# Optimization experiments

Hardware: AMD Instinct MI355X
Metric: run time of the kernel (lower is better)

The kernel has to match this reference:

```python
import jax, jax.numpy as jnp
import numpy as np
from jax import lax

B, T, X_DIM, HID, VOCAB = 64, 32, 512, 512, 10000


def setup_inputs() -> dict:
    key = jax.random.key(0)
    ks = jax.random.split(key, 20)
    s = 0.1
    inp = {
        "x": jax.random.normal(ks[0], (B, T, X_DIM), dtype=jnp.float32),
        "h": jax.random.normal(ks[1], (B, HID), dtype=jnp.float32),
        "c": jax.random.normal(ks[2], (B, HID), dtype=jnp.float32),
        "W_hi": jax.random.normal(ks[3], (HID, HID), dtype=jnp.float32) * s,
        "W_xi": jax.random.normal(ks[4], (X_DIM, HID), dtype=jnp.float32) * s,
        "b_i": jnp.zeros((HID,), dtype=jnp.float32),
        "W_hf": jax.random.normal(ks[5], (HID, HID), dtype=jnp.float32) * s,
        "W_xf": jax.random.normal(ks[6], (X_DIM, HID), dtype=jnp.float32) * s,
        "b_f": jnp.zeros((HID,), dtype=jnp.float32),
        "W_ho": jax.random.normal(ks[7], (HID, HID), dtype=jnp.float32) * s,
        "W_xo": jax.random.normal(ks[8], (X_DIM, HID), dtype=jnp.float32) * s,
        "b_o": jnp.zeros((HID,), dtype=jnp.float32),
        "W_hz": jax.random.normal(ks[9], (HID, HID), dtype=jnp.float32) * s,
        "W_xz": jax.random.normal(ks[10], (X_DIM, HID), dtype=jnp.float32) * s,
        "b_z": jnp.zeros((HID,), dtype=jnp.float32),
        # per-timestep Linear(hidden, vocab) bank: [T, HID, VOCAB] (y = h @ W + b)
        "W_lin": jax.random.normal(ks[11], (T, HID, VOCAB), dtype=jnp.float32) * 0.02,
        "b_lin": jnp.zeros((T, VOCAB), dtype=jnp.float32),
        # global embedding_layer: vocab -> x_dim
        "emb": jax.random.normal(ks[12], (VOCAB, X_DIM), dtype=jnp.float32) * 0.02,
    }
    return inp


def reference(x, h, c, W_hi, W_xi, b_i, W_hf, W_xf, b_f,
              W_ho, W_xo, b_o, W_hz, W_xz, b_z, W_lin, b_lin, emb):
    T_ = x.shape[1]
    # Faithful to the source: step 0 uses linear_list[0], then the loop over
    # t in range(T-1) uses linear_list[t] -> indices [0, 0, 1, ..., T-2].
    lin_idx = jnp.concatenate([jnp.zeros((1,), jnp.int32), jnp.arange(T_ - 1, dtype=jnp.int32)])
    Wl = W_lin[lin_idx]  # [T, HID, VOCAB]
    bl = b_lin[lin_idx]  # [T, VOCAB]

    def cell(x_in, h, c):
        i = jax.nn.sigmoid(h @ W_hi + x_in @ W_xi + b_i)
        f = jax.nn.sigmoid(h @ W_hf + x_in @ W_xf + b_f)
        o = jax.nn.sigmoid(h @ W_ho + x_in @ W_xo + b_o)
        z = jnp.tanh(h @ W_hz + x_in @ W_xz + b_z)
        c = i * z + f * c
        h = o * jnp.tanh(c)
        return h, c

    def step(carry, wb):
        h, c, x_in = carry
        Wt, bt = wb
        h, c = cell(x_in, h, c)
        y = jax.nn.softmax(h @ Wt + bt, axis=-1)  # [B, VOCAB]
        tok = jnp.argmax(y, axis=-1)              # [B]
        x_next = emb[tok]                         # [B, X_DIM]
        return (h, c, x_next), (y, c)

    # Only x[:, 0] is consumed (decoder feeds back argmax embeddings).
    (_, _, _), (ys, cs) = lax.scan(step, (h, c, x[:, 0]), (Wl, bl))
    outputs = jnp.transpose(ys, (1, 0, 2))      # [B, T, VOCAB]
    cell_states = jnp.transpose(cs, (1, 0, 2))  # [B, T, HID]
    return outputs, cell_states
```

## Files before the change

kernel.cpp:

```cpp
#include <hip/hip_runtime.h>
#include <hip/hip_bf16.h>
#include <stdint.h>

#define BB 64
#define TT 32
#define HID 512
#define XD  512
#define NV  10000

#define GRID   512
#define NCELL  128
#define VB     32
#define NLOG   313
#define LOGB   128
#define NORMB  441

typedef __bf16 bf16x8 __attribute__((ext_vector_type(8)));
typedef float  f32x4  __attribute__((ext_vector_type(4)));
typedef unsigned u32x4 __attribute__((ext_vector_type(4)));

__device__ inline void split2(float w, __bf16& hi, __bf16& lo) {
  hi = (__bf16)w;
  lo = (__bf16)(w - (float)hi);
}

__device__ inline unsigned long long shflxor64(unsigned long long v, int m) {
  unsigned lo = (unsigned)(v & 0xFFFFFFFFull);
  unsigned hi = (unsigned)(v >> 32);
  lo = __shfl_xor(lo, m);
  hi = __shfl_xor(hi, m);
  return ((unsigned long long)hi << 32) | lo;
}

__device__ inline unsigned long long packkey(float f, int v) {
  unsigned ub = __float_as_uint(f);
  unsigned key = (ub & 0x80000000u) ? ~ub : (ub | 0x80000000u);
  return ((unsigned long long)key << 32) | (unsigned)(0xFFFFFFFFu - (unsigned)v);
}

__device__ inline void st_wt16(void* addr, u32x4 d) {
  asm volatile("global_store_dwordx4 %0, %1, off sc0 sc1"
               :: "v"(addr), "v"(d) : "memory");
}

__device__ inline void spinP(int* base, int target) {
  if (threadIdx.x < 64) {
    int lane = threadIdx.x;
    int s;
    do {
      int v = 0;
      if (lane < 16)
        v = __hip_atomic_load(base + lane * 16, __ATOMIC_RELAXED,
                              __HIP_MEMORY_SCOPE_AGENT);
      #pragma unroll
      for (int m = 1; m < 16; m <<= 1) v += __shfl_xor(v, m);
      s = __shfl(v, 0);
      if (s < target) __builtin_amdgcn_s_sleep(1);
    } while (s < target);
  }
  __syncthreads();
}
__device__ inline void publish(int* base) {
  asm volatile("s_waitcnt vmcnt(0)" ::: "memory");
  __syncthreads();
  if (threadIdx.x == 0)
    __hip_atomic_fetch_add(base + (blockIdx.x & 15) * 16, 1,
                           __ATOMIC_RELAXED, __HIP_MEMORY_SCOPE_AGENT);
}

struct Params {
  const float *x, *emb;
  const float *Whi, *Whf, *Who, *Whz;
  const float *Wxi, *Wxf, *Wxo, *Wxz;
  const float *bi, *bfg, *bo, *bz;
  const float *W_lin, *b_lin;
  float* out;
  char* hb;
  char* xb;
  float* c_ws;
  float* psum;
  unsigned long long* pmax;
  float* inv;
  int* ctr;
};

__device__ inline void loadH(const char* hb, int tt, int row, int kk,
                             bf16x8& ah, bf16x8& al) {
  size_t off = (((size_t)tt * 128 + (kk >> 2)) * 64 + row) * 16;
  uint4 v0 = *(const uint4*)(hb + off);
  uint4 v1 = *(const uint4*)(hb + off + 1024);
  union { unsigned u[4]; bf16x8 v; } A, B;
  A.u[0] = v0.x; A.u[1] = v0.y; A.u[2] = v1.x; A.u[3] = v1.y;
  B.u[0] = v0.z; B.u[1] = v0.w; B.u[2] = v1.z; B.u[3] = v1.w;
  ah = A.v; al = B.v;
}

struct SMCell { __bf16 Ch[16][1042]; __bf16 Cl[16][1042]; float pre[64][17]; };
struct SMLog  { __bf16 Bh[32][522];  __bf16 Bl[32][522]; };
union SMU { SMCell c; SMLog l; };

__global__ __launch_bounds__(256) void k_init(
    const float* __restrict__ h0, const float* __restrict__ c0,
    char* __restrict__ hb, float* __restrict__ c_ws, int* __restrict__ ctrs) {
  int i = blockIdx.x * 256 + threadIdx.x;
  int row = i >> 9, k = i & 511, g = k >> 2, q = k & 3;
  float h = h0[i];
  __bf16 hi, lo; split2(h, hi, lo);
  char* base = hb + (((size_t)g) * 64 + row) * 16;
  ((unsigned short*)base)[q]       = __builtin_bit_cast(unsigned short, hi);
  ((unsigned short*)(base + 8))[q] = __builtin_bit_cast(unsigned short, lo);
  c_ws[i] = c0[i];
  if (i < 3 * TT * 256) ctrs[i] = 0;
}

__global__ __launch_bounds__(256, 2) void k_main(Params p) {
  __shared__ SMU sm;
  __shared__ float red_s[4];
  __shared__ unsigned long long red_m[4];
  __shared__ unsigned sh_tok;
  const int bid = blockIdx.x, tid = threadIdx.x;
  const int lane = tid & 63, wid = tid >> 6;

  int* cd0 = p.ctr;
  int* ld0 = p.ctr + TT * 256;
  int* rn0 = p.ctr + 2 * TT * 256;

  if (bid < NCELL) {
    const int n0 = bid * 4;
    const float* WH[4] = {p.Whi, p.Whf, p.Who, p.Whz};
    const float* WX[4] = {p.Wxi, p.Wxf, p.Wxo, p.Wxz};

    #pragma unroll
    for (int i2 = 0; i2 < 16; i2++) {
      int e = tid + i2 * 256;
      int k = e >> 2, g = e & 3;
      const float* src = (k < HID) ? (WH[g] + (size_t)k * HID + n0)
                                   : (WX[g] + (size_t)(k - HID) * HID + n0);
      float4 w = *(const float4*)src;
      #pragma unroll
      for (int j = 0; j < 4; j++) {
        __bf16 hi, lo; split2(((const float*)&w)[j], hi, lo);
        sm.c.Ch[g * 4 + j][k] = hi;
        sm.c.Cl[g * 4 + j][k] = lo;
      }
    }
    __syncthreads();

    const int row  = wid * 16 + (lane & 15);
    const int brow = lane & 15;

    for (int t = 0; t < TT; t++) {
      if (t > 0) spinP(cd0 + (t - 1) * 256, NCELL);

      f32x4 accA = {0.f, 0.f, 0.f, 0.f};
      f32x4 accB = {0.f, 0.f, 0.f, 0.f};

      #pragma unroll
      for (int ks = 0; ks < 16; ks++) {
        int kk = ks * 32 + (lane >> 4) * 8;
        bf16x8 ah, al;
        loadH(p.hb, t, row, kk, ah, al);
        bf16x8 bh = *(const bf16x8*)&sm.c.Ch[brow][kk];
        bf16x8 bl = *(const bf16x8*)&sm.c.Cl[brow][kk];
        accA = __builtin_amdgcn_mfma_f32_16x16x32_bf16(ah, bh, accA, 0, 0, 0);
        accB = __builtin_amdgcn_mfma_f32_16x16x32_bf16(ah, bl, accB, 0, 0, 0);
        accB = __builtin_amdgcn_mfma_f32_16x16x32_bf16(al, bh, accB, 0, 0, 0);
        accA = __builtin_amdgcn_mfma_f32_16x16x32_bf16(al, bl, accA, 0, 0, 0);
      }

      if (t == 0) {
        const float* xrow = p.x + (size_t)row * TT * XD;
        #pragma unroll
        for (int ks = 16; ks < 32; ks++) {
          int kk = ks * 32 + (lane >> 4) * 8;
          const float* xp = xrow + (kk - HID);
          float4 w0 = *(const float4*)(xp);
          float4 w1 = *(const float4*)(xp + 4);
          bf16x8 ah, al;
          #pragma unroll
          for (int j = 0; j < 4; j++) {
            __bf16 hi, lo;
            split2(((const float*)&w0)[j], hi, lo); ah[j] = hi; al[j] = lo;
            split2(((const float*)&w1)[j], hi, lo); ah[4 + j] = hi; al[4 + j] = lo;
          }
          bf16x8 bh = *(const bf16x8*)&sm.c.Ch[brow][kk];
          bf16x8 bl = *(const bf16x8*)&sm.c.Cl[brow][kk];
          accA = __builtin_amdgcn_mfma_f32_16x16x32_bf16(ah, bh, accA, 0, 0, 0);
          accB = __builtin_amdgcn_mfma_f32_16x16x32_bf16(ah, bl, accB, 0, 0, 0);
          accB = __builtin_amdgcn_mfma_f32_16x16x32_bf16(al, bh, accB, 0, 0, 0);
          accA = __builtin_amdgcn_mfma_f32_16x16x32_bf16(al, bl, accA, 0, 0, 0);
        }
      } else {
        spinP(rn0 + (t - 1) * 256, BB);
        #pragma unroll
        for (int ks = 16; ks < 32; ks++) {
          int kk = ks * 32 + (lane >> 4) * 8;
          bf16x8 ah, al;
          loadH(p.xb, t - 1, row, kk - 512, ah, al);
          bf16x8 bh = *(const bf16x8*)&sm.c.Ch[brow][kk];
          bf16x8 bl = *(const bf16x8*)&sm.c.Cl[brow][kk];
          accA = __builtin_amdgcn_mfma_f32_16x16x32_bf16(ah, bh, accA, 0, 0, 0);
          accB = __builtin_amdgcn_mfma_f32_16x16x32_bf16(ah, bl, accB, 0, 0, 0);
          accB = __builtin_amdgcn_mfma_f32_16x16x32_bf16(al, bh, accB, 0, 0, 0);
          accA = __builtin_amdgcn_mfma_f32_16x16x32_bf16(al, bl, accA, 0, 0, 0);
        }
      }

      #pragma unroll
      for (int j = 0; j < 4; j++)
        sm.c.pre[wid * 16 + (lane >> 4) * 4 + j][lane & 15] = accA[j] + accB[j];
      __syncthreads();

      float cnv; int rl, nn;
      {
        int rloc = tid >> 2, q = tid & 3;
        int n = n0 + q;
        float pi = sm.c.pre[rloc][q]      + p.bi[n];
        float pf = sm.c.pre[rloc][4 + q]  + p.bfg[n];
        float pq = sm.c.pre[rloc][8 + q]  + p.bo[n];
        float pz = sm.c.pre[rloc][12 + q] + p.bz[n];
        float ig = 1.f / (1.f + expf(-pi));
        float fg = 1.f / (1.f + expf(-pf));
        float og = 1.f / (1.f + expf(-pq));
        float zg = tanhf(pz);
        float cp = p.c_ws[rloc * HID + n];
        float cn = ig * zg + fg * cp;
        float hn = og * tanhf(cn);
        __bf16 hh, hl; split2(hn, hh, hl);
        unsigned hhu = (unsigned)__builtin_bit_cast(unsigned short, hh);
        unsigned hlu = (unsigned)__builtin_bit_cast(unsigned short, hl);
        unsigned hi1 = __shfl_down(hhu, 1), hi2 = __shfl_down(hhu, 2),
                 hi3 = __shfl_down(hhu, 3);
        unsigned lo1 = __shfl_down(hlu, 1), lo2 = __shfl_down(hlu, 2),
                 lo3 = __shfl_down(hlu, 3);
        if (q == 0) {
          u32x4 d = { hhu | (hi1 << 16), hi2 | (hi3 << 16),
                      hlu | (lo1 << 16), lo2 | (lo3 << 16) };
          st_wt16(p.hb + (((size_t)(t + 1) * 128 + bid) * 64 + rloc) * 16, d);
        }
        cnv = cn; rl = rloc; nn = n;
      }
      publish(cd0 + t * 256);
      p.c_ws[rl * HID + nn] = cnv;
      p.out[(size_t)BB * TT * NV + (size_t)rl * TT * HID + (size_t)t * HID + nn] = cnv;
    }
    return;
  }

  if (bid < NORMB) {
    const int lb = bid - LOGB;
    const int v0 = lb * VB;
    const int row = wid * 16 + (lane & 15);

    float bcar[2];
    float evp[2][4];

    auto stageW = [&](int widx) {
      const float* W = p.W_lin + (size_t)widx * HID * NV;
      float4 v[16];
      #pragma unroll
      for (int i2 = 0; i2 < 16; i2++) {
        int e = tid + i2 * 256;
        int k = e >> 3, pp = e & 7;
        v[i2] = *(const float4*)(W + (size_t)k * NV + v0 + pp * 4);
      }
      const float* bn = p.b_lin + (size_t)widx * NV;
      bcar[0] = bn[v0 + (lane & 15)];
      bcar[1] = bn[v0 + 16 + (lane & 15)];
      #pragma unroll
      for (int i2 = 0; i2 < 16; i2++) {
        int e = tid + i2 * 256;
        int k = e >> 3, pp = e & 7;
        #pragma unroll
        for (int j = 0; j < 4; j++) {
          __bf16 hi, lo; split2(((const float*)&v[i2])[j], hi, lo);
          sm.l.Bh[pp * 4 + j][k] = hi;
          sm.l.Bl[pp * 4 + j][k] = lo;
        }
      }
    };

    stageW(0);

    for (int t = 0; t < TT; t++) {
      spinP(cd0 + t * 256, NCELL);

      f32x4 acc[2][2] = {};
      #pragma unroll
      for (int ks = 0; ks < 16; ks++) {
        int kk = ks * 32 + (lane >> 4) * 8;
        bf16x8 ah, al;
        loadH(p.hb, t + 1, row, kk, ah, al);
        #pragma unroll
        for (int vt = 0; vt < 2; vt++) {
          int rrow = vt * 16 + (lane & 15);
          bf16x8 bh = *(const bf16x8*)&sm.l.Bh[rrow][kk];
          bf16x8 bl = *(const bf16x8*)&sm.l.Bl[rrow][kk];
          acc[vt][0] = __builtin_amdgcn_mfma_f32_16x16x32_bf16(ah, bh, acc[vt][0], 0, 0, 0);
          acc[vt][1] = __builtin_amdgcn_mfma_f32_16x16x32_bf16(ah, bl, acc[vt][1], 0, 0, 0);
          acc[vt][1] = __builtin_amdgcn_mfma_f32_16x16x32_bf16(al, bh, acc[vt][1], 0, 0, 0);
          acc[vt][0] = __builtin_amdgcn_mfma_f32_16x16x32_bf16(al, bl, acc[vt][0], 0, 0, 0);
        }
      }

      float ev[2][4];
      float rsum[4] = {0.f, 0.f, 0.f, 0.f};
      unsigned long long rmax[4] = {0ULL, 0ULL, 0ULL, 0ULL};
      #pragma unroll
      for (int vt = 0; vt < 2; vt++) {
        int v = v0 + vt * 16 + (lane & 15);
        bool ok = (v < NV);
        float bb = ok ? bcar[vt] : 0.f;
        #pragma unroll
        for (int j = 0; j < 4; j++) {
          float logit = acc[vt][0][j] + acc[vt][1][j] + bb;
          float e = ok ? expf(logit) : 0.f;
          ev[vt][j] = e;
          rsum[j] += e;
          if (ok) {
            unsigned long long pk = packkey(logit, v);
            if (pk > rmax[j]) rmax[j] = pk;
          }
        }
      }

      #pragma unroll
      for (int off = 1; off < 16; off <<= 1) {
        #pragma unroll
        for (int j = 0; j < 4; j++) {
          rsum[j] += __shfl_xor(rsum[j], off);
          unsigned long long o = shflxor64(rmax[j], off);
          if (o > rmax[j]) rmax[j] = o;
        }
      }
      if ((lane & 15) == 0) {
        int rbase = wid * 16 + (lane >> 4) * 4;
        union { float f[4]; u32x4 u; } S;
        S.f[0] = rsum[0]; S.f[1] = rsum[1]; S.f[2] = rsum[2]; S.f[3] = rsum[3];
        st_wt16(&p.psum[((size_t)t * NLOG + lb) * 64 + rbase], S.u);
        u32x4 M0 = { (unsigned)rmax[0], (unsigned)(rmax[0] >> 32),
                     (unsigned)rmax[1], (unsigned)(rmax[1] >> 32) };
        u32x4 M1 = { (unsigned)rmax[2], (unsigned)(rmax[2] >> 32),
                     (unsigned)rmax[3], (unsigned)(rmax[3] >> 32) };
        st_wt16(&p.pmax[((size_t)t * NLOG + lb) * 64 + rbase], M0);
        st_wt16(&p.pmax[((size_t)t * NLOG + lb) * 64 + rbase + 2], M1);
      }
      publish(ld0 + t * 256);

      if (t < TT - 1) stageW(t);

      if (t > 0) {
        float invr[4];
        #pragma unroll
        for (int j = 0; j < 4; j++)
          invr[j] = p.inv[(size_t)(t - 1) * BB + wid * 16 + (lane >> 4) * 4 + j];
        #pragma unroll
        for (int vt = 0; vt < 2; vt++) {
          int v = v0 + vt * 16 + (lane & 15);
          if (v < NV) {
            #pragma unroll
            for (int j = 0; j < 4; j++) {
              int r = wid * 16 + (lane >> 4) * 4 + j;
              p.out[(size_t)r * TT * NV + (size_t)(t - 1) * NV + v] = evp[vt][j] * invr[j];
            }
          }
        }
      }
      #pragma unroll
      for (int vt = 0; vt < 2; vt++)
        #pragma unroll
        for (int j = 0; j < 4; j++) evp[vt][j] = ev[vt][j];
    }

    spinP(rn0 + (TT - 1) * 256, BB);
    float invr[4];
    #pragma unroll
    for (int j = 0; j < 4; j++)
      invr[j] = p.inv[(size_t)(TT - 1) * BB + wid * 16 + (lane >> 4) * 4 + j];
    #pragma unroll
    for (int vt = 0; vt < 2; vt++) {
      int v = v0 + vt * 16 + (lane & 15);
      if (v < NV) {
        #pragma unroll
        for (int j = 0; j < 4; j++) {
          int r = wid * 16 + (lane >> 4) * 4 + j;
          p.out[(size_t)r * TT * NV + (size_t)(TT - 1) * NV + v] = evp[vt][j] * invr[j];
        }
      }
    }
    return;
  }

  if (bid < NORMB + BB) {
    const int r = bid - NORMB;
    for (int t = 0; t < TT; t++) {
      spinP(ld0 + t * 256, NLOG);

      float s = 0.f; unsigned long long m = 0ULL;
      for (int i = tid; i < NLOG; i += 256) {
        s += p.psum[((size_t)t * NLOG + i) * 64 + r];
        unsigned long long v = p.pmax[((size_t)t * NLOG + i) * 64 + r];
        if (v > m) m = v;
      }
      #pragma unroll
      for (int off = 1; off < 64; off <<= 1) {
        s += __shfl_xor(s, off);
        unsigned long long o = shflxor64(m, off);
        if (o > m) m = o;
      }
      if (lane == 0) { red_s[wid] = s; red_m[wid] = m; }
      __syncthreads();
      if (tid == 0) {
        s = red_s[0] + red_s[1] + red_s[2] + red_s[3];
        m = red_m[0];
        if (red_m[1] > m) m = red_m[1];
        if (red_m[2] > m) m = red_m[2];
        if (red_m[3] > m) m = red_m[3];
        sh_tok = 0xFFFFFFFFu - (unsigned)(m & 0xFFFFFFFFull);
        __hip_atomic_store(&p.inv[(size_t)t * BB + r], 1.0f / s,
                           __ATOMIC_RELAXED, __HIP_MEMORY_SCOPE_AGENT);
      }
      __syncthreads();

      unsigned tokv = sh_tok;
      if (tid < 128) {
        float4 w = *(const float4*)(p.emb + (size_t)tokv * XD + tid * 4);
        unsigned h[4], l[4];
        #pragma unroll
        for (int j = 0; j < 4; j++) {
          __bf16 hi, lo; split2(((const float*)&w)[j], hi, lo);
          h[j] = (unsigned)__builtin_bit_cast(unsigned short, hi);
          l[j] = (unsigned)__builtin_bit_cast(unsigned short, lo);
        }
        u32x4 d = { h[0] | (h[1] << 16), h[2] | (h[3] << 16),
                    l[0] | (l[1] << 16), l[2] | (l[3] << 16) };
        st_wt16(p.xb + (((size_t)t * 128 + tid) * 64 + r) * 16, d);
      }
      publish(rn0 + t * 256);
      __syncthreads();
    }
    return;
  }
}

extern "C" void kernel_launch(void* const* d_in, const int* in_sizes, int n_in,
                              void* d_out, int out_size, void* d_ws, size_t ws_size,
                              hipStream_t stream) {
  const float* x     = (const float*)d_in[0];
  const float* h0    = (const float*)d_in[1];
  const float* c0    = (const float*)d_in[2];
  const float* W_hi  = (const float*)d_in[3];
  const float* W_xi  = (const float*)d_in[4];
  const float* b_i   = (const float*)d_in[5];
  const float* W_hf  = (const float*)d_in[6];
  const float* W_xf  = (const float*)d_in[7];
  const float* b_f   = (const float*)d_in[8];
  const float* W_ho  = (const float*)d_in[9];
  const float* W_xo  = (const float*)d_in[10];
  const float* b_o   = (const float*)d_in[11];
  const float* W_hz  = (const float*)d_in[12];
  const float* W_xz  = (const float*)d_in[13];
  const float* b_z   = (const float*)d_in[14];
  const float* W_lin = (const float*)d_in[15];
  const float* b_lin = (const float*)d_in[16];
  const float* emb   = (const float*)d_in[17];

  float* out = (float*)d_out;
  char* ws = (char*)d_ws;
  char*   hb   = ws;
  char*   xb   = ws + 4325376;
  float*  c_ws = (float*)(ws + 8519680);
  float*  psum = (float*)(ws + 8650752);
  unsigned long long* pmax = (unsigned long long*)(ws + 11214848);
  float*  inv  = (float*)(ws + 16343040);
  int*    ctrs = (int*)(ws + 16351232);

  k_init<<<128, 256, 0, stream>>>(h0, c0, hb, c_ws, ctrs);

  Params P;
  P.x = x; P.emb = emb;
  P.Whi = W_hi; P.Whf = W_hf; P.Who = W_ho; P.Whz = W_hz;
  P.Wxi = W_xi; P.Wxf = W_xf; P.Wxo = W_xo; P.Wxz = W_xz;
  P.bi = b_i; P.bfg = b_f; P.bo = b_o; P.bz = b_z;
  P.W_lin = W_lin; P.b_lin = b_lin;
  P.out = out;
  P.hb = hb; P.xb = xb; P.c_ws = c_ws;
  P.psum = psum; P.pmax = pmax; P.inv = inv;
  P.ctr = ctrs;

  k_main<<<GRID, 256, 0, stream>>>(P);
}
```

Baseline: 818.3 us.

## Publish argmax tokens and gather embeddings in cell blocks; prefetch W_lin before publish

```diff
diff --git a/kernel.cpp b/kernel.cpp
--- a/kernel.cpp
+++ b/kernel.cpp
@@ -76,10 +76,10 @@
   const float *W_lin, *b_lin;
   float* out;
   char* hb;
-  char* xb;
   float* c_ws;
   float* psum;
   unsigned long long* pmax;
+  unsigned* tok;
   float* inv;
   int* ctr;
 };
@@ -117,7 +117,6 @@
   __shared__ SMU sm;
   __shared__ float red_s[4];
   __shared__ unsigned long long red_m[4];
-  __shared__ unsigned sh_tok;
   const int bid = blockIdx.x, tid = threadIdx.x;
   const int lane = tid & 63, wid = tid >> 6;
 
@@ -168,42 +167,34 @@
         accA = __builtin_amdgcn_mfma_f32_16x16x32_bf16(al, bl, accA, 0, 0, 0);
       }
 
+      const float* xrow;
       if (t == 0) {
-        const float* xrow = p.x + (size_t)row * TT * XD;
-        #pragma unroll
-        for (int ks = 16; ks < 32; ks++) {
-          int kk = ks * 32 + (lane >> 4) * 8;
-          const float* xp = xrow + (kk - HID);
-          float4 w0 = *(const float4*)(xp);
-          float4 w1 = *(const float4*)(xp + 4);
-          bf16x8 ah, al;
-          #pragma unroll
-          for (int j = 0; j < 4; j++) {
-            __bf16 hi, lo;
-            split2(((const float*)&w0)[j], hi, lo); ah[j] = hi; al[j] = lo;
-            split2(((const float*)&w1)[j], hi, lo); ah[4 + j] = hi; al[4 + j] = lo;
-          }
-          bf16x8 bh = *(const bf16x8*)&sm.c.Ch[brow][kk];
-          bf16x8 bl = *(const bf16x8*)&sm.c.Cl[brow][kk];
-          accA = __builtin_amdgcn_mfma_f32_16x16x32_bf16(ah, bh, accA, 0, 0, 0);
-          accB = __builtin_amdgcn_mfma_f32_16x16x32_bf16(ah, bl, accB, 0, 0, 0);
-          accB = __builtin_amdgcn_mfma_f32_16x16x32_bf16(al, bh, accB, 0, 0, 0);
-          accA = __builtin_amdgcn_mfma_f32_16x16x32_bf16(al, bl, accA, 0, 0, 0);
-        }
+        xrow = p.x + (size_t)row * TT * XD;
       } else {
         spinP(rn0 + (t - 1) * 256, BB);
-        #pragma unroll
-        for (int ks = 16; ks < 32; ks++) {
-          int kk = ks * 32 + (lane >> 4) * 8;
-          bf16x8 ah, al;
-          loadH(p.xb, t - 1, row, kk - 512, ah, al);
-          bf16x8 bh = *(const bf16x8*)&sm.c.Ch[brow][kk];
-          bf16x8 bl = *(const bf16x8*)&sm.c.Cl[brow][kk];
-          accA = __builtin_amdgcn_mfma_f32_16x16x32_bf16(ah, bh, accA, 0, 0, 0);
-          accB = __builtin_amdgcn_mfma_f32_16x16x32_bf16(ah, bl, accB, 0, 0, 0);
-          accB = __builtin_amdgcn_mfma_f32_16x16x32_bf16(al, bh, accB, 0, 0, 0);
-          accA = __builtin_amdgcn_mfma_f32_16x16x32_bf16(al, bl, accA, 0, 0, 0);
-        }
+        unsigned tokv = p.tok[(size_t)(t - 1) * BB + row];
+        xrow = p.emb + (size_t)tokv * XD;
+      }
+
+      #pragma unroll
+      for (int ks = 16; ks < 32; ks++) {
+        int kk = ks * 32 + (lane >> 4) * 8;
+        const float* xp = xrow + (kk - HID);
+        float4 w0 = *(const float4*)(xp);
+        float4 w1 = *(const float4*)(xp + 4);
+        bf16x8 ah, al;
+        #pragma unroll
+        for (int j = 0; j < 4; j++) {
+          __bf16 hi, lo;
+          split2(((const float*)&w0)[j], hi, lo); ah[j] = hi; al[j] = lo;
+          split2(((const float*)&w1)[j], hi, lo); ah[4 + j] = hi; al[4 + j] = lo;
+        }
+        bf16x8 bh = *(const bf16x8*)&sm.c.Ch[brow][kk];
+        bf16x8 bl = *(const bf16x8*)&sm.c.Cl[brow][kk];
+        accA = __builtin_amdgcn_mfma_f32_16x16x32_bf16(ah, bh, accA, 0, 0, 0);
+        accB = __builtin_amdgcn_mfma_f32_16x16x32_bf16(ah, bl, accB, 0, 0, 0);
+        accB = __builtin_amdgcn_mfma_f32_16x16x32_bf16(al, bh, accB, 0, 0, 0);
+        accA = __builtin_amdgcn_mfma_f32_16x16x32_bf16(al, bl, accA, 0, 0, 0);
       }
 
       #pragma unroll
@@ -255,15 +246,16 @@
     float bcar[2];
     float evp[2][4];
 
-    auto stageW = [&](int widx) {
+    auto issueW = [&](int widx, float4* v) {
       const float* W = p.W_lin + (size_t)widx * HID * NV;
-      float4 v[16];
       #pragma unroll
       for (int i2 = 0; i2 < 16; i2++) {
         int e = tid + i2 * 256;
         int k = e >> 3, pp = e & 7;
         v[i2] = *(const float4*)(W + (size_t)k * NV + v0 + pp * 4);
       }
+    };
+    auto convertW = [&](int widx, float4* v) {
       const float* bn = p.b_lin + (size_t)widx * NV;
       bcar[0] = bn[v0 + (lane & 15)];
       bcar[1] = bn[v0 + 16 + (lane & 15)];
@@ -280,10 +272,15 @@
       }
     };
 
-    stageW(0);
+    {
+      float4 v[16];
+      issueW(0, v);
+      convertW(0, v);
+    }
 
     for (int t = 0; t < TT; t++) {
       spinP(cd0 + t * 256, NCELL);
+      asm volatile("s_waitcnt vmcnt(0)" ::: "memory");
 
       f32x4 acc[2][2] = {};
       #pragma unroll
@@ -345,9 +342,19 @@
         st_wt16(&p.pmax[((size_t)t * NLOG + lb) * 64 + rbase], M0);
         st_wt16(&p.pmax[((size_t)t * NLOG + lb) * 64 + rbase + 2], M1);
       }
-      publish(ld0 + t * 256);
-
-      if (t < TT - 1) stageW(t);
+      float4 v[16];
+      if (t < TT - 1) {
+        issueW(t, v);
+        asm volatile("s_waitcnt vmcnt(16)" ::: "memory");
+      } else {
+        asm volatile("s_waitcnt vmcnt(0)" ::: "memory");
+      }
+      __syncthreads();
+      if (tid == 0)
+        __hip_atomic_fetch_add(ld0 + t * 256 + (bid & 15) * 16, 1,
+                               __ATOMIC_RELAXED, __HIP_MEMORY_SCOPE_AGENT);
+
+      if (t < TT - 1) convertW(t, v);
 
       if (t > 0) {
         float invr[4];
@@ -416,25 +423,11 @@
         if (red_m[1] > m) m = red_m[1];
         if (red_m[2] > m) m = red_m[2];
         if (red_m[3] > m) m = red_m[3];
-        sh_tok = 0xFFFFFFFFu - (unsigned)(m & 0xFFFFFFFFull);
+        __hip_atomic_store(&p.tok[(size_t)t * BB + r],
+                           0xFFFFFFFFu - (unsigned)(m & 0xFFFFFFFFull),
+                           __ATOMIC_RELAXED, __HIP_MEMORY_SCOPE_AGENT);
         __hip_atomic_store(&p.inv[(size_t)t * BB + r], 1.0f / s,
                            __ATOMIC_RELAXED, __HIP_MEMORY_SCOPE_AGENT);
-      }
-      __syncthreads();
-
-      unsigned tokv = sh_tok;
-      if (tid < 128) {
-        float4 w = *(const float4*)(p.emb + (size_t)tokv * XD + tid * 4);
-        unsigned h[4], l[4];
-        #pragma unroll
-        for (int j = 0; j < 4; j++) {
-          __bf16 hi, lo; split2(((const float*)&w)[j], hi, lo);
-          h[j] = (unsigned)__builtin_bit_cast(unsigned short, hi);
-          l[j] = (unsigned)__builtin_bit_cast(unsigned short, lo);
-        }
-        u32x4 d = { h[0] | (h[1] << 16), h[2] | (h[3] << 16),
-                    l[0] | (l[1] << 16), l[2] | (l[3] << 16) };
-        st_wt16(p.xb + (((size_t)t * 128 + tid) * 64 + r) * 16, d);
       }
       publish(rn0 + t * 256);
       __syncthreads();
@@ -468,12 +461,12 @@
   float* out = (float*)d_out;
   char* ws = (char*)d_ws;
   char*   hb   = ws;
-  char*   xb   = ws + 4325376;
-  float*  c_ws = (float*)(ws + 8519680);
-  float*  psum = (float*)(ws + 8650752);
-  unsigned long long* pmax = (unsigned long long*)(ws + 11214848);
-  float*  inv  = (float*)(ws + 16343040);
-  int*    ctrs = (int*)(ws + 16351232);
+  float*  c_ws = (float*)(ws + 4325376);
+  float*  psum = (float*)(ws + 4456448);
+  unsigned long long* pmax = (unsigned long long*)(ws + 7020544);
+  unsigned* tok = (unsigned*)(ws + 12148736);
+  float*  inv  = (float*)(ws + 12156928);
+  int*    ctrs = (int*)(ws + 12165120);
 
   k_init<<<128, 256, 0, stream>>>(h0, c0, hb, c_ws, ctrs);
 
@@ -484,8 +477,8 @@
   P.bi = b_i; P.bfg = b_f; P.bo = b_o; P.bz = b_z;
   P.W_lin = W_lin; P.b_lin = b_lin;
   P.out = out;
-  P.hb = hb; P.xb = xb; P.c_ws = c_ws;
-  P.psum = psum; P.pmax = pmax; P.inv = inv;
+  P.hb = hb; P.c_ws = c_ws;
+  P.psum = psum; P.pmax = pmax; P.tok = tok; P.inv = inv;
   P.ctr = ctrs;
 
   k_main<<<GRID, 256, 0, stream>>>(P);
```

Result: slower. 1.083 ms (+32.3%).

## Widen counter striping for barriers and keep cell state in registers

Applied to the files above, without the earlier changes.

```diff
diff --git a/kernel.cpp b/kernel.cpp
--- a/kernel.cpp
+++ b/kernel.cpp
@@ -43,33 +43,35 @@
                :: "v"(addr), "v"(d) : "memory");
 }
 
-__device__ inline void spinP(int* base, int target) {
+template<int NL>
+__device__ inline void spinN(int* base, int target) {
   if (threadIdx.x < 64) {
     int lane = threadIdx.x;
     int s;
     do {
       int v = 0;
-      if (lane < 16)
+      if (NL >= 64 || lane < NL)
         v = __hip_atomic_load(base + lane * 16, __ATOMIC_RELAXED,
                               __HIP_MEMORY_SCOPE_AGENT);
       #pragma unroll
-      for (int m = 1; m < 16; m <<= 1) v += __shfl_xor(v, m);
-      s = __shfl(v, 0);
+      for (int m = 1; m < 64; m <<= 1) v += __shfl_xor(v, m);
+      s = v;
       if (s < target) __builtin_amdgcn_s_sleep(1);
     } while (s < target);
   }
   __syncthreads();
 }
-__device__ inline void publish(int* base) {
+template<int NL>
+__device__ inline void publishN(int* base) {
   asm volatile("s_waitcnt vmcnt(0)" ::: "memory");
   __syncthreads();
   if (threadIdx.x == 0)
-    __hip_atomic_fetch_add(base + (blockIdx.x & 15) * 16, 1,
+    __hip_atomic_fetch_add(base + (blockIdx.x & (NL - 1)) * 16, 1,
                            __ATOMIC_RELAXED, __HIP_MEMORY_SCOPE_AGENT);
 }
 
 struct Params {
-  const float *x, *emb;
+  const float *x, *emb, *c0;
   const float *Whi, *Whf, *Who, *Whz;
   const float *Wxi, *Wxf, *Wxo, *Wxz;
   const float *bi, *bfg, *bo, *bz;
@@ -77,7 +79,6 @@
   float* out;
   char* hb;
   char* xb;
-  float* c_ws;
   float* psum;
   unsigned long long* pmax;
   float* inv;
@@ -99,9 +100,11 @@
 struct SMLog  { __bf16 Bh[32][522];  __bf16 Bl[32][522]; };
 union SMU { SMCell c; SMLog l; };
 
+#define CTR_TOTAL (TT * 512 + TT * 1024 + TT * 256)
+
 __global__ __launch_bounds__(256) void k_init(
-    const float* __restrict__ h0, const float* __restrict__ c0,
-    char* __restrict__ hb, float* __restrict__ c_ws, int* __restrict__ ctrs) {
+    const float* __restrict__ h0,
+    char* __restrict__ hb, int* __restrict__ ctrs) {
   int i = blockIdx.x * 256 + threadIdx.x;
   int row = i >> 9, k = i & 511, g = k >> 2, q = k & 3;
   float h = h0[i];
@@ -109,8 +112,7 @@
   char* base = hb + (((size_t)g) * 64 + row) * 16;
   ((unsigned short*)base)[q]       = __builtin_bit_cast(unsigned short, hi);
   ((unsigned short*)(base + 8))[q] = __builtin_bit_cast(unsigned short, lo);
-  c_ws[i] = c0[i];
-  if (i < 3 * TT * 256) ctrs[i] = 0;
+  for (int j = i; j < CTR_TOTAL; j += 128 * 256) ctrs[j] = 0;
 }
 
 __global__ __launch_bounds__(256, 2) void k_main(Params p) {
@@ -122,8 +124,8 @@
   const int lane = tid & 63, wid = tid >> 6;
 
   int* cd0 = p.ctr;
-  int* ld0 = p.ctr + TT * 256;
-  int* rn0 = p.ctr + 2 * TT * 256;
+  int* ld0 = p.ctr + TT * 512;
+  int* rn0 = p.ctr + TT * 512 + TT * 1024;
 
   if (bid < NCELL) {
     const int n0 = bid * 4;
@@ -148,9 +150,11 @@
 
     const int row  = wid * 16 + (lane & 15);
     const int brow = lane & 15;
+    const int rl0  = tid >> 2, nn0 = n0 + (tid & 3);
+    float creg = p.c0[rl0 * HID + nn0];
 
     for (int t = 0; t < TT; t++) {
-      if (t > 0) spinP(cd0 + (t - 1) * 256, NCELL);
+      if (t > 0) spinN<32>(cd0 + (t - 1) * 512, NCELL);
 
       f32x4 accA = {0.f, 0.f, 0.f, 0.f};
       f32x4 accB = {0.f, 0.f, 0.f, 0.f};
@@ -191,7 +195,7 @@
           accA = __builtin_amdgcn_mfma_f32_16x16x32_bf16(al, bl, accA, 0, 0, 0);
         }
       } else {
-        spinP(rn0 + (t - 1) * 256, BB);
+        spinN<16>(rn0 + (t - 1) * 256, BB);
         #pragma unroll
         for (int ks = 16; ks < 32; ks++) {
           int kk = ks * 32 + (lane >> 4) * 8;
@@ -211,20 +215,18 @@
         sm.c.pre[wid * 16 + (lane >> 4) * 4 + j][lane & 15] = accA[j] + accB[j];
       __syncthreads();
 
-      float cnv; int rl, nn;
+      float cnv;
       {
-        int rloc = tid >> 2, q = tid & 3;
-        int n = n0 + q;
-        float pi = sm.c.pre[rloc][q]      + p.bi[n];
-        float pf = sm.c.pre[rloc][4 + q]  + p.bfg[n];
-        float pq = sm.c.pre[rloc][8 + q]  + p.bo[n];
-        float pz = sm.c.pre[rloc][12 + q] + p.bz[n];
+        float pi = sm.c.pre[rl0][(tid & 3)]      + p.bi[nn0];
+        float pf = sm.c.pre[rl0][4 + (tid & 3)]  + p.bfg[nn0];
+        float pq = sm.c.pre[rl0][8 + (tid & 3)]  + p.bo[nn0];
+        float pz = sm.c.pre[rl0][12 + (tid & 3)] + p.bz[nn0];
         float ig = 1.f / (1.f + expf(-pi));
         float fg = 1.f / (1.f + expf(-pf));
         float og = 1.f / (1.f + expf(-pq));
         float zg = tanhf(pz);
-        float cp = p.c_ws[rloc * HID + n];
-        float cn = ig * zg + fg * cp;
+        float cn = ig * zg + fg * creg;
+        creg = cn;
         float hn = og * tanhf(cn);
         __bf16 hh, hl; split2(hn, hh, hl);
         unsigned hhu = (unsigned)__builtin_bit_cast(unsigned short, hh);
@@ -233,16 +235,15 @@
                  hi3 = __shfl_down(hhu, 3);
         unsigned lo1 = __shfl_down(hlu, 1), lo2 = __shfl_down(hlu, 2),
                  lo3 = __shfl_down(hlu, 3);
-        if (q == 0) {
+        if ((tid & 3) == 0) {
           u32x4 d = { hhu | (hi1 << 16), hi2 | (hi3 << 16),
                       hlu | (lo1 << 16), lo2 | (lo3 << 16) };
-          st_wt16(p.hb + (((size_t)(t + 1) * 128 + bid) * 64 + rloc) * 16, d);
-        }
-        cnv = cn; rl = rloc; nn = n;
-      }
-      publish(cd0 + t * 256);
-      p.c_ws[rl * HID + nn] = cnv;
-      p.out[(size_t)BB * TT * NV + (size_t)rl * TT * HID + (size_t)t * HID + nn] = cnv;
+          st_wt16(p.hb + (((size_t)(t + 1) * 128 + bid) * 64 + rl0) * 16, d);
+        }
+        cnv = cn;
+      }
+      publishN<32>(cd0 + t * 512);
+      p.out[(size_t)BB * TT * NV + (size_t)rl0 * TT * HID + (size_t)t * HID + nn0] = cnv;
     }
     return;
   }
@@ -283,7 +284,7 @@
     stageW(0);
 
     for (int t = 0; t < TT; t++) {
-      spinP(cd0 + t * 256, NCELL);
+      spinN<32>(cd0 + t * 512, NCELL);
 
       f32x4 acc[2][2] = {};
       #pragma unroll
@@ -345,7 +346,7 @@
         st_wt16(&p.pmax[((size_t)t * NLOG + lb) * 64 + rbase], M0);
         st_wt16(&p.pmax[((size_t)t * NLOG + lb) * 64 + rbase + 2], M1);
       }
-      publish(ld0 + t * 256);
+      publishN<64>(ld0 + t * 1024);
 
       if (t < TT - 1) stageW(t);
 
@@ -372,7 +373,7 @@
         for (int j = 0; j < 4; j++) evp[vt][j] = ev[vt][j];
     }
 
-    spinP(rn0 + (TT - 1) * 256, BB);
+    spinN<16>(rn0 + (TT - 1) * 256, BB);
     float invr[4];
     #pragma unroll
     for (int j = 0; j < 4; j++)
@@ -394,7 +395,7 @@
   if (bid < NORMB + BB) {
     const int r = bid - NORMB;
     for (int t = 0; t < TT; t++) {
-      spinP(ld0 + t * 256, NLOG);
+      spinN<64>(ld0 + t * 1024, NLOG);
 
       float s = 0.f; unsigned long long m = 0ULL;
       for (int i = tid; i < NLOG; i += 256) {
@@ -417,7 +418,8 @@
         if (red_m[2] > m) m = red_m[2];
         if (red_m[3] > m) m = red_m[3];
         sh_tok = 0xFFFFFFFFu - (unsigned)(m & 0xFFFFFFFFull);
-        __hip_atomic_store(&p.inv[(size_t)t * BB + r], 1.0f / s,
+        __hip_atomic_store((unsigned*)&p.inv[(size_t)t * BB + r],
+                           __builtin_bit_cast(unsigned, 1.0f / s),
                            __ATOMIC_RELAXED, __HIP_MEMORY_SCOPE_AGENT);
       }
       __syncthreads();
@@ -436,7 +438,7 @@
                     l[0] | (l[1] << 16), l[2] | (l[3] << 16) };
         st_wt16(p.xb + (((size_t)t * 128 + tid) * 64 + r) * 16, d);
       }
-      publish(rn0 + t * 256);
+      publishN<16>(rn0 + t * 256);
       __syncthreads();
     }
     return;
@@ -469,22 +471,21 @@
   char* ws = (char*)d_ws;
   char*   hb   = ws;
   char*   xb   = ws + 4325376;
-  float*  c_ws = (float*)(ws + 8519680);
-  float*  psum = (float*)(ws + 8650752);
-  unsigned long long* pmax = (unsigned long long*)(ws + 11214848);
-  float*  inv  = (float*)(ws + 16343040);
-  int*    ctrs = (int*)(ws + 16351232);
-
-  k_init<<<128, 256, 0, stream>>>(h0, c0, hb, c_ws, ctrs);
+  float*  psum = (float*)(ws + 8519680);
+  unsigned long long* pmax = (unsigned long long*)(ws + 11083776);
+  float*  inv  = (float*)(ws + 16211968);
+  int*    ctrs = (int*)(ws + 16220160);
+
+  k_init<<<128, 256, 0, stream>>>(h0, hb, ctrs);
 
   Params P;
-  P.x = x; P.emb = emb;
+  P.x = x; P.emb = emb; P.c0 = c0;
   P.Whi = W_hi; P.Whf = W_hf; P.Who = W_ho; P.Whz = W_hz;
   P.Wxi = W_xi; P.Wxf = W_xf; P.Wxo = W_xo; P.Wxz = W_xz;
   P.bi = b_i; P.bfg = b_f; P.bo = b_o; P.bz = b_z;
   P.W_lin = W_lin; P.b_lin = b_lin;
   P.out = out;
-  P.hb = hb; P.xb = xb; P.c_ws = c_ws;
+  P.hb = hb; P.xb = xb;
   P.psum = psum; P.pmax = pmax; P.inv = inv;
   P.ctr = ctrs;
 
```

Result: faster. 746.8 us (-8.7%).
